# Kernel optimization log

Measured on AMD Instinct MI355X. Metric: run time of the kernel, lower is better.

## Reference

```python
import jax, jax.numpy as jnp
import numpy as np

B, CIN, COUT, H, W = 16, 128, 128, 64, 64
K1, K2, DIL = 3, 3, 1
PAD0 = DIL * (K1 - 1) // 2
PAD1 = DIL * (K2 - 1) // 2
L = H * W


def setup_inputs() -> dict:
    key = jax.random.key(0)
    k1, k2, k3, k4, k5 = jax.random.split(key, 5)
    x = jax.random.normal(k1, (B, CIN, H, W), dtype=jnp.float32)
    # binary per-pixel mask over kernel taps, broadcast over batch*channels
    mask = (jax.random.uniform(k2, (1, K1 * K2, L)) < 0.5).astype(jnp.float32)
    fan_in = CIN * K1 * K2
    bound = 1.0 / np.sqrt(fan_in)
    weight = jax.random.uniform(k3, (COUT, CIN, K1, K2), jnp.float32, -bound, bound)
    mask_weight = jax.random.uniform(k4, (COUT, K1, K2), jnp.float32, -bound, bound)
    bias = jax.random.uniform(k5, (COUT,), jnp.float32, -bound, bound)
    return {"x": x, "mask": mask, "weight": weight, "mask_weight": mask_weight, "bias": bias}


def reference(x, mask, weight, mask_weight, bias):
    # im2col: [B, CIN*K1*K2, H, W]; channel ordering (cin, k1, k2) matches torch unfold
    patches = jax.lax.conv_general_dilated_patches(
        x, (K1, K2), (1, 1), [(PAD0, PAD0), (PAD1, PAD1)], rhs_dilation=(DIL, DIL))
    p = patches.reshape(B, CIN, K1 * K2, L)
    p = p * mask[:, None, :, :]          # mask [1, K, L] broadcasts over B and CIN
    p = p.reshape(B, CIN * K1 * K2, L)
    out = jnp.einsum('ok,bkl->bol', weight.reshape(COUT, -1), p)
    out = out + bias[None, :, None]
    out = out + jnp.einsum('ok,mkl->mol', mask_weight.reshape(COUT, -1), mask)
    return out.reshape(B, COUT, H, W)
```

## Files before the change

kernel.cpp:

```cpp
#include <hip/hip_runtime.h>
#include <stdint.h>

#define B_    16
#define CIN_  128
#define COUT_ 128
#define H_    64
#define W_    64
#define L_    4096
#define KK_   1152
#define PW_   66
#define PPIX_ (PW_ * PW_)

typedef unsigned short u16;
typedef __bf16 bf16x8 __attribute__((ext_vector_type(8)));
typedef float  floatx4 __attribute__((ext_vector_type(4)));
typedef uint32_t u32x4 __attribute__((ext_vector_type(4)));

typedef const __attribute__((address_space(1))) uint32_t* gptr_t;
typedef __attribute__((address_space(3))) uint32_t*       lptr_t;

__device__ __forceinline__ void async_copy16(const void* g, void* l) {
    __builtin_amdgcn_global_load_lds((gptr_t)g, (lptr_t)l, 16, 0, 0);
}

__device__ __forceinline__ u16 f2bf(float f) {
    uint32_t u = __builtin_bit_cast(uint32_t, f);
    uint32_t r = u + 0x7FFFu + ((u >> 16) & 1u);
    return (u16)(r >> 16);
}

__global__ void lmc_transpose_kernel(const float* __restrict__ x, u16* __restrict__ xTp) {
    __shared__ u16 tile[64][CIN_ + 8];
    const int b   = blockIdx.y;
    const int y   = blockIdx.x;
    const int tid = threadIdx.x;

    {
        const int c  = tid >> 1;
        const int x0 = (tid & 1) * 32;
        const float* src = x + ((size_t)b * CIN_ + c) * L_ + y * 64 + x0;
        #pragma unroll
        for (int j = 0; j < 32; j += 4) {
            float4 v = *reinterpret_cast<const float4*>(src + j);
            tile[x0 + j + 0][c] = f2bf(v.x);
            tile[x0 + j + 1][c] = f2bf(v.y);
            tile[x0 + j + 2][c] = f2bf(v.z);
            tile[x0 + j + 3][c] = f2bf(v.w);
        }
    }
    __syncthreads();

    u16* dstrow = xTp + ((size_t)(b * PW_ + (y + 1)) * PW_) * CIN_;
    {
        const int xx   = tid >> 2;
        const int cseg = (tid & 3) * 32;
        u16* dst = dstrow + (size_t)(xx + 1) * CIN_ + cseg;
        #pragma unroll
        for (int i = 0; i < 32; i += 8) {
            *reinterpret_cast<uint4*>(dst + i) =
                *reinterpret_cast<const uint4*>(&tile[xx][cseg + i]);
        }
    }
    const uint4 z = {0u, 0u, 0u, 0u};
    if (tid < 32) {
        const int pix = (tid >> 4) ? 65 : 0;
        *reinterpret_cast<uint4*>(dstrow + (size_t)pix * CIN_ + (tid & 15) * 8) = z;
    }
    if (y == 0 || y == 63) {
        u16* brow = xTp + ((size_t)(b * PW_ + (y == 0 ? 0 : 65)) * PW_) * CIN_;
        for (int i = tid; i < (PW_ * CIN_) / 8; i += 256)
            reinterpret_cast<uint4*>(brow)[i] = z;
    }
}

__global__ void lmc_prep_kernel(const float* __restrict__ mask, const float* __restrict__ mw,
                                const float* __restrict__ bias, const float* __restrict__ w,
                                float* __restrict__ mb, u16* __restrict__ wb2) {
    const int bid = blockIdx.x, tid = threadIdx.x;
    if (bid < 128) {
        const int o = bid;
        float m[9];
        #pragma unroll
        for (int k = 0; k < 9; ++k) m[k] = mw[o * 9 + k];
        const float bs = bias[o];
        for (int l = tid; l < L_; l += 256) {
            float s = bs;
            #pragma unroll
            for (int k = 0; k < 9; ++k) s += m[k] * mask[k * L_ + l];
            mb[o * L_ + l] = s;
        }
    } else {
        const int base = (bid - 128) * 2304;
        #pragma unroll
        for (int i = 0; i < 9; ++i) {
            const int e = base + i * 256 + tid;
            const int k = e >> 14;
            const int rem = e & 16383;
            const int o = rem >> 7, c = rem & 127;
            wb2[e] = f2bf(w[(size_t)o * KK_ + c * 9 + k]);
        }
    }
}

__global__ __launch_bounds__(512, 2)
void lmc_gemm_kernel(const u16* __restrict__ xTp, const u16* __restrict__ wb2,
                     const float* __restrict__ mask, const float* __restrict__ mb,
                     float* __restrict__ out) {
    __shared__ u16 W_lds[396 * 128];

    const int flat    = blockIdx.x;
    const int logical = (flat & 7) * 32 + (flat >> 3);
    const int b       = logical >> 4;
    const int lt      = logical & 15;
    const int Y       = lt * 4;
    const int l0      = lt * 256;

    const int tid  = threadIdx.x;
    const int lane = tid & 63;
    const int wv   = tid >> 6;
    const int wm   = (wv >> 2) * 64;
    const int wn   = (wv & 3) * 64;
    const int lrow = lane & 15;
    const int quad = lane >> 4;

    {
        const char* xw = (const char*)xTp + ((size_t)(b * PW_ + Y) * PW_) * 256;
        for (int t = wv; t < 99; t += 8) {
            const int p    = t * 4 + quad;
            const int srcc = lrow ^ (p & 7);
            async_copy16(xw + (size_t)p * 256 + srcc * 16,
                         (char*)W_lds + t * 1024);
        }
    }

    int arow[4];
    #pragma unroll
    for (int i = 0; i < 4; ++i)
        arow[i] = (wm + i * 16 + lrow) * 128 + quad * 8;

    bf16x8 af[4][4];
    #pragma unroll
    for (int i = 0; i < 4; ++i)
        #pragma unroll
        for (int ks = 0; ks < 4; ++ks)
            af[i][ks] = *reinterpret_cast<const bf16x8*>(wb2 + arow[i] + ks * 32);

    int pix0[4];
    uint64_t bits = 0;
    #pragma unroll
    for (int j = 0; j < 4; ++j) {
        const int ll = wn + j * 16 + lrow;
        pix0[j] = ((ll >> 6) + 1) * 66 + (ll & 63) + 1;
        const int lg = l0 + ll;
        #pragma unroll
        for (int k = 0; k < 9; ++k)
            if (mask[k * L_ + lg] != 0.0f) bits |= (1ull << (k * 4 + j));
    }

    floatx4 acc[4][4];
    #pragma unroll
    for (int i = 0; i < 4; ++i)
        #pragma unroll
        for (int j = 0; j < 4; ++j)
            acc[i][j] = (floatx4){0.f, 0.f, 0.f, 0.f};

    __syncthreads();

    for (int k = 0; k < 9; ++k) {
        const int dy = k / 3 - 1;
        const int dx = k - (k / 3) * 3 - 1;
        const int sh = dy * 66 + dx;
        const int kn = (k < 8) ? k + 1 : 8;
        const u16* wkn = wb2 + kn * 16384;

        uint32_t kp[4];
        #pragma unroll
        for (int j = 0; j < 4; ++j)
            kp[j] = 0u - (uint32_t)((bits >> (k * 4 + j)) & 1ull);

        #pragma unroll
        for (int ks = 0; ks < 4; ++ks) {
            bf16x8 bfr[4];
            #pragma unroll
            for (int j = 0; j < 4; ++j) {
                const int pix  = pix0[j] + sh;
                const int slot = (ks * 4 + quad) ^ (pix & 7);
                bf16x8 v = *reinterpret_cast<const bf16x8*>(&W_lds[pix * 128 + slot * 8]);
                u32x4 t = __builtin_bit_cast(u32x4, v);
                t &= kp[j];
                bfr[j] = __builtin_bit_cast(bf16x8, t);
            }
            #pragma unroll
            for (int i = 0; i < 4; ++i)
                #pragma unroll
                for (int j = 0; j < 4; ++j)
                    acc[i][j] = __builtin_amdgcn_mfma_f32_16x16x32_bf16(af[i][ks], bfr[j], acc[i][j], 0, 0, 0);
            #pragma unroll
            for (int i = 0; i < 4; ++i)
                af[i][ks] = *reinterpret_cast<const bf16x8*>(wkn + arow[i] + ks * 32);
        }
    }

    #pragma unroll
    for (int i = 0; i < 4; ++i) {
        #pragma unroll
        for (int j = 0; j < 4; ++j) {
            const int l = l0 + wn + j * 16 + lrow;
            #pragma unroll
            for (int r = 0; r < 4; ++r) {
                const int o = wm + i * 16 + quad * 4 + r;
                out[((size_t)b * COUT_ + o) * L_ + l] = acc[i][j][r] + mb[o * L_ + l];
            }
        }
    }
}

extern "C" void kernel_launch(void* const* d_in, const int* in_sizes, int n_in,
                              void* d_out, int out_size, void* d_ws, size_t ws_size,
                              hipStream_t stream) {
    const float* x      = (const float*)d_in[0];
    const float* mask   = (const float*)d_in[1];
    const float* weight = (const float*)d_in[2];
    const float* mw     = (const float*)d_in[3];
    const float* bias   = (const float*)d_in[4];
    float* out = (float*)d_out;

    char* ws = (char*)d_ws;
    u16*   xTp = (u16*)ws;
    u16*   wb2 = (u16*)(ws + 17842176);
    float* mb  = (float*)(ws + 17842176 + 294912);

    lmc_transpose_kernel<<<dim3(64, B_), 256, 0, stream>>>(x, xTp);
    lmc_prep_kernel<<<192, 256, 0, stream>>>(mask, mw, bias, weight, mb, wb2);
    lmc_gemm_kernel<<<dim3(256), 512, 0, stream>>>(xTp, wb2, mask, mb, out);
}
```

Before: 143.3 us.

## Merge prep kernels, halve GEMM tile, double-buffer LDS B fragments

Folds the transpose kernel into the prep kernel so one launch covers the input transpose, the mask-bias precompute and the weight reorder. The GEMM block shrinks from 512 to 256 threads covering 2 image rows (128 pixels) per block, giving 512 blocks and a smaller LDS footprint. The inner loop is unrolled with ping-pong B-fragment registers so LDS reads for the next k-step are issued before the current MFMAs. This aims to cut launch overhead, improve occupancy and load balance, and hide LDS latency. The cost is more halo rows loaded per output pixel and higher register pressure from the double buffers.

```diff
diff --git a/kernel.cpp b/kernel.cpp
--- a/kernel.cpp
+++ b/kernel.cpp
@@ -29,56 +29,55 @@
     return (u16)(r >> 16);
 }
 
-__global__ void lmc_transpose_kernel(const float* __restrict__ x, u16* __restrict__ xTp) {
-    __shared__ u16 tile[64][CIN_ + 8];
-    const int b   = blockIdx.y;
-    const int y   = blockIdx.x;
-    const int tid = threadIdx.x;
-
-    {
-        const int c  = tid >> 1;
-        const int x0 = (tid & 1) * 32;
-        const float* src = x + ((size_t)b * CIN_ + c) * L_ + y * 64 + x0;
-        #pragma unroll
-        for (int j = 0; j < 32; j += 4) {
-            float4 v = *reinterpret_cast<const float4*>(src + j);
-            tile[x0 + j + 0][c] = f2bf(v.x);
-            tile[x0 + j + 1][c] = f2bf(v.y);
-            tile[x0 + j + 2][c] = f2bf(v.z);
-            tile[x0 + j + 3][c] = f2bf(v.w);
-        }
-    }
-    __syncthreads();
-
-    u16* dstrow = xTp + ((size_t)(b * PW_ + (y + 1)) * PW_) * CIN_;
-    {
-        const int xx   = tid >> 2;
-        const int cseg = (tid & 3) * 32;
-        u16* dst = dstrow + (size_t)(xx + 1) * CIN_ + cseg;
-        #pragma unroll
-        for (int i = 0; i < 32; i += 8) {
-            *reinterpret_cast<uint4*>(dst + i) =
-                *reinterpret_cast<const uint4*>(&tile[xx][cseg + i]);
-        }
-    }
-    const uint4 z = {0u, 0u, 0u, 0u};
-    if (tid < 32) {
-        const int pix = (tid >> 4) ? 65 : 0;
-        *reinterpret_cast<uint4*>(dstrow + (size_t)pix * CIN_ + (tid & 15) * 8) = z;
-    }
-    if (y == 0 || y == 63) {
-        u16* brow = xTp + ((size_t)(b * PW_ + (y == 0 ? 0 : 65)) * PW_) * CIN_;
-        for (int i = tid; i < (PW_ * CIN_) / 8; i += 256)
-            reinterpret_cast<uint4*>(brow)[i] = z;
-    }
-}
-
-__global__ void lmc_prep_kernel(const float* __restrict__ mask, const float* __restrict__ mw,
+__global__ void lmc_prep_kernel(const float* __restrict__ x,
+                                const float* __restrict__ mask, const float* __restrict__ mw,
                                 const float* __restrict__ bias, const float* __restrict__ w,
-                                float* __restrict__ mb, u16* __restrict__ wb2) {
+                                u16* __restrict__ xTp, float* __restrict__ mb,
+                                u16* __restrict__ wb2) {
     const int bid = blockIdx.x, tid = threadIdx.x;
-    if (bid < 128) {
-        const int o = bid;
+    if (bid < 1024) {
+        __shared__ u16 tile[64][CIN_ + 8];
+        const int b = bid >> 6;
+        const int y = bid & 63;
+
+        {
+            const int c  = tid >> 1;
+            const int x0 = (tid & 1) * 32;
+            const float* src = x + ((size_t)b * CIN_ + c) * L_ + y * 64 + x0;
+            #pragma unroll
+            for (int j = 0; j < 32; j += 4) {
+                float4 v = *reinterpret_cast<const float4*>(src + j);
+                tile[x0 + j + 0][c] = f2bf(v.x);
+                tile[x0 + j + 1][c] = f2bf(v.y);
+                tile[x0 + j + 2][c] = f2bf(v.z);
+                tile[x0 + j + 3][c] = f2bf(v.w);
+            }
+        }
+        __syncthreads();
+
+        u16* dstrow = xTp + ((size_t)(b * PW_ + (y + 1)) * PW_) * CIN_;
+        {
+            const int xx   = tid >> 2;
+            const int cseg = (tid & 3) * 32;
+            u16* dst = dstrow + (size_t)(xx + 1) * CIN_ + cseg;
+            #pragma unroll
+            for (int i = 0; i < 32; i += 8) {
+                *reinterpret_cast<uint4*>(dst + i) =
+                    *reinterpret_cast<const uint4*>(&tile[xx][cseg + i]);
+            }
+        }
+        const uint4 z = {0u, 0u, 0u, 0u};
+        if (tid < 32) {
+            const int pix = (tid >> 4) ? 65 : 0;
+            *reinterpret_cast<uint4*>(dstrow + (size_t)pix * CIN_ + (tid & 15) * 8) = z;
+        }
+        if (y == 0 || y == 63) {
+            u16* brow = xTp + ((size_t)(b * PW_ + (y == 0 ? 0 : 65)) * PW_) * CIN_;
+            for (int i = tid; i < (PW_ * CIN_) / 8; i += 256)
+                reinterpret_cast<uint4*>(brow)[i] = z;
+        }
+    } else if (bid < 1152) {
+        const int o = bid - 1024;
         float m[9];
         #pragma unroll
         for (int k = 0; k < 9; ++k) m[k] = mw[o * 9 + k];
@@ -90,7 +89,7 @@
             mb[o * L_ + l] = s;
         }
     } else {
-        const int base = (bid - 128) * 2304;
+        const int base = (bid - 1152) * 2304;
         #pragma unroll
         for (int i = 0; i < 9; ++i) {
             const int e = base + i * 256 + tid;
@@ -102,30 +101,63 @@
     }
 }
 
-__global__ __launch_bounds__(512, 2)
+#define SH_(k) (((k) / 3 - 1) * 66 + ((k) % 3 - 1))
+
+#define GSTEP(cur, nxt, k, ks, DO_LOAD, kn, ksn)                              \
+    do {                                                                      \
+        if (DO_LOAD) {                                                        \
+            const int shn = SH_(kn);                                          \
+            _Pragma("unroll")                                                 \
+            for (int j = 0; j < 4; ++j) {                                     \
+                const int pixn  = pix0[j] + shn;                              \
+                const int slotn = ((ksn) * 4 + quad) ^ (pixn & 7);            \
+                nxt[j] = *reinterpret_cast<const bf16x8*>(                    \
+                            &W_lds[pixn * 128 + slotn * 8]);                  \
+            }                                                                 \
+        }                                                                     \
+        bf16x8 bm[4];                                                         \
+        _Pragma("unroll")                                                     \
+        for (int j = 0; j < 4; ++j) {                                         \
+            u32x4 t = __builtin_bit_cast(u32x4, cur[j]);                      \
+            t &= kp[j];                                                       \
+            bm[j] = __builtin_bit_cast(bf16x8, t);                            \
+        }                                                                     \
+        _Pragma("unroll")                                                     \
+        for (int i = 0; i < 4; ++i)                                           \
+            _Pragma("unroll")                                                 \
+            for (int j = 0; j < 4; ++j)                                       \
+                acc[i][j] = __builtin_amdgcn_mfma_f32_16x16x32_bf16(          \
+                    af[i][ks], bm[j], acc[i][j], 0, 0, 0);                    \
+        _Pragma("unroll")                                                     \
+        for (int i = 0; i < 4; ++i)                                           \
+            af[i][ks] = *reinterpret_cast<const bf16x8*>(                     \
+                wkn + arow[i] + (ks) * 32);                                   \
+    } while (0)
+
+__global__ __launch_bounds__(256, 2)
 void lmc_gemm_kernel(const u16* __restrict__ xTp, const u16* __restrict__ wb2,
                      const float* __restrict__ mask, const float* __restrict__ mb,
                      float* __restrict__ out) {
-    __shared__ u16 W_lds[396 * 128];
+    __shared__ u16 W_lds[264 * 128];
 
     const int flat    = blockIdx.x;
-    const int logical = (flat & 7) * 32 + (flat >> 3);
-    const int b       = logical >> 4;
-    const int lt      = logical & 15;
-    const int Y       = lt * 4;
-    const int l0      = lt * 256;
+    const int logical = (flat & 7) * 64 + (flat >> 3);
+    const int b       = logical >> 5;
+    const int lt      = logical & 31;
+    const int Y       = lt * 2;
+    const int l0      = lt * 128;
 
     const int tid  = threadIdx.x;
     const int lane = tid & 63;
     const int wv   = tid >> 6;
-    const int wm   = (wv >> 2) * 64;
-    const int wn   = (wv & 3) * 64;
+    const int wm   = (wv >> 1) * 64;
+    const int wn   = (wv & 1) * 64;
     const int lrow = lane & 15;
     const int quad = lane >> 4;
 
     {
         const char* xw = (const char*)xTp + ((size_t)(b * PW_ + Y) * PW_) * 256;
-        for (int t = wv; t < 99; t += 8) {
+        for (int t = wv; t < 66; t += 4) {
             const int p    = t * 4 + quad;
             const int srcc = lrow ^ (p & 7);
             async_copy16(xw + (size_t)p * 256 + srcc * 16,
@@ -166,39 +198,29 @@
 
     __syncthreads();
 
+    bf16x8 bA[4], bB[4];
+    {
+        const int sh0 = SH_(0);
+        #pragma unroll
+        for (int j = 0; j < 4; ++j) {
+            const int pix  = pix0[j] + sh0;
+            const int slot = quad ^ (pix & 7);
+            bA[j] = *reinterpret_cast<const bf16x8*>(&W_lds[pix * 128 + slot * 8]);
+        }
+    }
+
+    #pragma unroll
     for (int k = 0; k < 9; ++k) {
-        const int dy = k / 3 - 1;
-        const int dx = k - (k / 3) * 3 - 1;
-        const int sh = dy * 66 + dx;
-        const int kn = (k < 8) ? k + 1 : 8;
-        const u16* wkn = wb2 + kn * 16384;
-
+        const u16* wkn = wb2 + ((k < 8) ? (k + 1) : 8) * 16384;
         uint32_t kp[4];
         #pragma unroll
         for (int j = 0; j < 4; ++j)
             kp[j] = 0u - (uint32_t)((bits >> (k * 4 + j)) & 1ull);
 
-        #pragma unroll
-        for (int ks = 0; ks < 4; ++ks) {
-            bf16x8 bfr[4];
-            #pragma unroll
-            for (int j = 0; j < 4; ++j) {
-                const int pix  = pix0[j] + sh;
-                const int slot = (ks * 4 + quad) ^ (pix & 7);
-                bf16x8 v = *reinterpret_cast<const bf16x8*>(&W_lds[pix * 128 + slot * 8]);
-                u32x4 t = __builtin_bit_cast(u32x4, v);
-                t &= kp[j];
-                bfr[j] = __builtin_bit_cast(bf16x8, t);
-            }
-            #pragma unroll
-            for (int i = 0; i < 4; ++i)
-                #pragma unroll
-                for (int j = 0; j < 4; ++j)
-                    acc[i][j] = __builtin_amdgcn_mfma_f32_16x16x32_bf16(af[i][ks], bfr[j], acc[i][j], 0, 0, 0);
-            #pragma unroll
-            for (int i = 0; i < 4; ++i)
-                af[i][ks] = *reinterpret_cast<const bf16x8*>(wkn + arow[i] + ks * 32);
-        }
+        GSTEP(bA, bB, k, 0, true,      k,     1);
+        GSTEP(bB, bA, k, 1, true,      k,     2);
+        GSTEP(bA, bB, k, 2, true,      k,     3);
+        GSTEP(bB, bA, k, 3, (k < 8),   k + 1, 0);
     }
 
     #pragma unroll
@@ -230,7 +252,6 @@
     u16*   wb2 = (u16*)(ws + 17842176);
     float* mb  = (float*)(ws + 17842176 + 294912);
 
-    lmc_transpose_kernel<<<dim3(64, B_), 256, 0, stream>>>(x, xTp);
-    lmc_prep_kernel<<<192, 256, 0, stream>>>(mask, mw, bias, weight, mb, wb2);
-    lmc_gemm_kernel<<<dim3(256), 512, 0, stream>>>(xTp, wb2, mask, mb, out);
-}
+    lmc_prep_kernel<<<1216, 256, 0, stream>>>(x, mask, mw, bias, weight, xTp, mb, wb2);
+    lmc_gemm_kernel<<<512, 256, 0, stream>>>(xTp, wb2, mask, mb, out);
+}
```

Measured after the change: 142.0 us. About the same (-0.9%).
